# Kernel optimization log

Measured on AMD Instinct MI355X. Metric: run time of the kernel, lower is better.

Reference implementation:

```python
import jax, jax.numpy as jnp
import numpy as np

N, E = 16384, 524288
IN_C, H1, H2 = 128, 128, 64
EDGE_F = 16
NB = 10                      # binary outputs
MC_GROUPS = (4, 6)           # multi-class group sizes (proto, service)
NC = 10                      # continuous outputs
EPS = 1e-5


def setup_inputs() -> dict:
    key = jax.random.key(0)
    ks = jax.random.split(key, 16)
    def lin(k, fan_in, fan_out):
        s = 1.0 / np.sqrt(fan_in)
        kw, kb = jax.random.split(k)
        return (jax.random.uniform(kw, (fan_in, fan_out), jnp.float32, -s, s),
                jax.random.uniform(kb, (fan_out,), jnp.float32, -s, s))
    w1, b1 = lin(ks[0], IN_C, H1)
    w2, b2 = lin(ks[1], H1, H2)
    w_bin, b_bin = lin(ks[2], H2, NB)
    w_mc, b_mc = lin(ks[3], H2, sum(MC_GROUPS))
    w_cont, b_cont = lin(ks[4], H2, NC)
    w_edge, b_edge = lin(ks[5], 2 * H2, EDGE_F)
    return {
        "x": jax.random.normal(ks[6], (N, IN_C), jnp.float32),
        "edge_index": jax.random.randint(ks[7], (2, E), 0, N, jnp.int64),
        "edge_attr": jax.random.normal(ks[8], (E, EDGE_F), jnp.float32),
        "w1": w1, "b1": b1,
        "bn1_g": jnp.ones((H1,), jnp.float32), "bn1_b": jnp.zeros((H1,), jnp.float32),
        "w2": w2, "b2": b2,
        "bn2_g": jnp.ones((H2,), jnp.float32), "bn2_b": jnp.zeros((H2,), jnp.float32),
        "w_bin": w_bin, "b_bin": b_bin,
        "w_mc": w_mc, "b_mc": b_mc,
        "w_cont": w_cont, "b_cont": b_cont,
        "w_edge": w_edge, "b_edge": b_edge,
    }


def _gcn(x, w, b, src, dst, norm, n):
    # GCNConv: x' = D^-1/2 (A+I) D^-1/2 (x W) + b
    h = x @ w
    msg = h[src] * norm[:, None]
    agg = jax.ops.segment_sum(msg, dst, num_segments=n)
    return agg + b


def _bn(h, g, b):
    m = jnp.mean(h, axis=0)
    v = jnp.var(h, axis=0)
    return g * (h - m) * jax.lax.rsqrt(v + EPS) + b


def reference(x, edge_index, edge_attr, w1, b1, bn1_g, bn1_b, w2, b2, bn2_g, bn2_b,
              w_bin, b_bin, w_mc, b_mc, w_cont, b_cont, w_edge, b_edge):
    n = x.shape[0]
    loops = jnp.arange(n, dtype=edge_index.dtype)
    src = jnp.concatenate([edge_index[0], loops])
    dst = jnp.concatenate([edge_index[1], loops])
    deg = jax.ops.segment_sum(jnp.ones_like(src, dtype=x.dtype), dst, num_segments=n)
    dis = jax.lax.rsqrt(deg)  # deg >= 1 thanks to self-loops
    norm = dis[src] * dis[dst]

    h = jax.nn.relu(_bn(_gcn(x, w1, b1, src, dst, norm, n), bn1_g, bn1_b))
    z = jax.nn.relu(_bn(_gcn(h, w2, b2, src, dst, norm, n), bn2_g, bn2_b))

    # node feature reconstruction: [binary sigmoid | per-group softmax | continuous]
    binary = jax.nn.sigmoid(z @ w_bin + b_bin)
    mc_logits = z @ w_mc + b_mc
    mc_parts, s = [], 0
    for g in MC_GROUPS:
        mc_parts.append(jax.nn.softmax(mc_logits[:, s:s + g], axis=1))
        s += g
    cont = z @ w_cont + b_cont
    reconstructed_x = jnp.concatenate([binary] + mc_parts + [cont], axis=1)

    adj = z @ z.T  # [N, N]

    edge_emb = jnp.concatenate([z[edge_index[0]], z[edge_index[1]]], axis=1)
    edge_features = edge_emb @ w_edge + b_edge
    return (reconstructed_x, adj, edge_features)
```

## Files before the change

### kernel.cpp

```cpp
#include <hip/hip_runtime.h>
#include <hip/hip_bf16.h>
#include <math.h>


constexpr int kN = 16384;
constexpr int kE = 524288;
constexpr float kEps = 1e-5f;

typedef __attribute__((ext_vector_type(8))) short short8v;
typedef __attribute__((ext_vector_type(4))) float f32x4;

__device__ inline float bf2f(unsigned short u) {
  return __uint_as_float(((unsigned)u) << 16);
}
__device__ inline unsigned short f2bf(float f) {
  unsigned u = __float_as_uint(f);
  return (unsigned short)((u + 0x7fff + ((u >> 16) & 1)) >> 16);
}

__global__ void zero_kernel(int* counts, float* sums1, float* sums2,
                            const float* __restrict__ we, __hip_bfloat16* wfr) {
  int i = blockIdx.x * 256 + threadIdx.x;
  if (i < kN) counts[i] = 0;
  if (i < 256) sums1[i] = 0.f;
  if (i < 128) sums2[i] = 0.f;
  if (i < 2048) {
    int f = i >> 9, l = (i >> 3) & 63, j = i & 7;
    int lr = l & 15, lg = l >> 4;
    int krow = f * 32 + lg * 8 + j;
    wfr[i] = __float2bfloat16(we[krow * 16 + lr]);
  }
}

__global__ void hist_kernel(const int* __restrict__ dst, int* __restrict__ counts) {
  int e = blockIdx.x * 256 + threadIdx.x;
  if (e < kE) atomicAdd(&counts[dst[e]], 1);
}

__global__ __launch_bounds__(1024) void scan_kernel(const int* __restrict__ counts,
    int* __restrict__ offsets, int* __restrict__ pos, float* __restrict__ dis) {
  __shared__ int wave_tot[16];
  int tid = threadIdx.x;
  int base = tid * 16;
  int loc[16];
  int s = 0;
#pragma unroll
  for (int i = 0; i < 16; i++) { loc[i] = s; s += counts[base + i]; }
  int lane = tid & 63, wv = tid >> 6;
  int incl = s;
#pragma unroll
  for (int d = 1; d < 64; d <<= 1) {
    int v = __shfl_up(incl, d, 64);
    if (lane >= d) incl += v;
  }
  if (lane == 63) wave_tot[wv] = incl;
  __syncthreads();
  int woff = 0;
  for (int i = 0; i < wv; i++) woff += wave_tot[i];
  int excl = woff + incl - s;
#pragma unroll
  for (int i = 0; i < 16; i++) {
    int o = excl + loc[i];
    offsets[base + i] = o;
    pos[base + i] = o;
    dis[base + i] = rsqrtf((float)counts[base + i] + 1.0f);
  }
}

__global__ void fill_kernel(const int* __restrict__ src, const int* __restrict__ dst,
                            int* __restrict__ pos, int* __restrict__ csr_src) {
  int e = blockIdx.x * 256 + threadIdx.x;
  if (e < kE) {
    int d = dst[e];
    int p = atomicAdd(&pos[d], 1);
    csr_src[p] = src[e];
  }
}

__global__ __launch_bounds__(256) void gemm1_kernel(
    const float* __restrict__ A, const float* __restrict__ W,
    const float* __restrict__ dis, __hip_bfloat16* __restrict__ out) {
  constexpr int BC = 128, NJ = 8, WF4 = 4;
  __shared__ float xs[64 * 33];
  __shared__ float wsh[32 * BC];
  int tid = threadIdx.x;
  int tx = tid & 15, ty = tid >> 4;
  int r0 = blockIdx.x * 64;
  float acc[4][NJ];
#pragma unroll
  for (int r = 0; r < 4; r++)
#pragma unroll
    for (int j = 0; j < NJ; j++) acc[r][j] = 0.f;

  for (int kb = 0; kb < 128; kb += 32) {
    __syncthreads();
#pragma unroll
    for (int q = 0; q < 2; q++) {
      int f = tid + q * 256;
      int row = f >> 3, kq = f & 7;
      float4 v = *(const float4*)(A + (size_t)(r0 + row) * 128 + kb + kq * 4);
      int bb = row * 33 + kq * 4;
      xs[bb + 0] = v.x; xs[bb + 1] = v.y; xs[bb + 2] = v.z; xs[bb + 3] = v.w;
    }
#pragma unroll
    for (int q = 0; q < WF4; q++) {
      int f = tid + q * 256;
      int k = f / (BC / 4), cq = f % (BC / 4);
      *(float4*)&wsh[k * BC + cq * 4] =
          *(const float4*)(W + (size_t)(kb + k) * BC + cq * 4);
    }
    __syncthreads();
#pragma unroll
    for (int kk = 0; kk < 32; kk++) {
      float av[4];
#pragma unroll
      for (int r = 0; r < 4; r++) av[r] = xs[(ty * 4 + r) * 33 + kk];
#pragma unroll
      for (int j = 0; j < NJ; j++) {
        float bv = wsh[kk * BC + tx + j * 16];
#pragma unroll
        for (int r = 0; r < 4; r++) acc[r][j] = fmaf(av[r], bv, acc[r][j]);
      }
    }
  }
#pragma unroll
  for (int r = 0; r < 4; r++) {
    int row = r0 + ty * 4 + r;
    float dr = dis[row];
#pragma unroll
    for (int j = 0; j < NJ; j++)
      out[(size_t)row * BC + tx + j * 16] = __float2bfloat16(acc[r][j] * dr);
  }
}

__global__ __launch_bounds__(256) void gemm2_kernel(
    const unsigned short* __restrict__ A, const float* __restrict__ W,
    const float* __restrict__ sums, const float* __restrict__ g,
    const float* __restrict__ b, const float* __restrict__ dis,
    __hip_bfloat16* __restrict__ out) {
  constexpr int BC = 64, NJ = 4, WF4 = 2;
  __shared__ float xs[64 * 33];
  __shared__ float wsh[32 * BC];
  __shared__ float s_scl[128], s_shf[128];
  int tid = threadIdx.x;
  if (tid < 128) {
    float mean = sums[tid] / (float)kN;
    float var = sums[128 + tid] / (float)kN - mean * mean;
    float inv = rsqrtf(var + kEps);
    float sc = g[tid] * inv;
    s_scl[tid] = sc;
    s_shf[tid] = b[tid] - mean * sc;
  }
  int tx = tid & 15, ty = tid >> 4;
  int r0 = blockIdx.x * 64;
  float acc[4][NJ];
#pragma unroll
  for (int r = 0; r < 4; r++)
#pragma unroll
    for (int j = 0; j < NJ; j++) acc[r][j] = 0.f;

  for (int kb = 0; kb < 128; kb += 32) {
    __syncthreads();
    {
      int row = tid >> 2, kq = tid & 3;
      short8v v8 = *(const short8v*)(A + (size_t)(r0 + row) * 128 + kb + kq * 8);
      int bb = row * 33 + kq * 8;
#pragma unroll
      for (int j = 0; j < 8; j++) {
        int c = kb + kq * 8 + j;
        float v = bf2f((unsigned short)v8[j]);
        xs[bb + j] = fmaxf(0.f, fmaf(v, s_scl[c], s_shf[c]));
      }
    }
#pragma unroll
    for (int q = 0; q < WF4; q++) {
      int f = tid + q * 256;
      int k = f / (BC / 4), cq = f % (BC / 4);
      *(float4*)&wsh[k * BC + cq * 4] =
          *(const float4*)(W + (size_t)(kb + k) * BC + cq * 4);
    }
    __syncthreads();
#pragma unroll
    for (int kk = 0; kk < 32; kk++) {
      float av[4];
#pragma unroll
      for (int r = 0; r < 4; r++) av[r] = xs[(ty * 4 + r) * 33 + kk];
#pragma unroll
      for (int j = 0; j < NJ; j++) {
        float bv = wsh[kk * BC + tx + j * 16];
#pragma unroll
        for (int r = 0; r < 4; r++) acc[r][j] = fmaf(av[r], bv, acc[r][j]);
      }
    }
  }
#pragma unroll
  for (int r = 0; r < 4; r++) {
    int row = r0 + ty * 4 + r;
    float dr = dis[row];
#pragma unroll
    for (int j = 0; j < NJ; j++)
      out[(size_t)row * BC + tx + j * 16] = __float2bfloat16(acc[r][j] * dr);
  }
}

__global__ __launch_bounds__(256) void agg1_kernel(const unsigned short* __restrict__ hs,
    const int* __restrict__ csr_src, const int* __restrict__ offsets,
    const int* __restrict__ counts, const float* __restrict__ dis,
    unsigned short* __restrict__ t1) {
  int tid = threadIdx.x;
  int wv = tid >> 6, lane = tid & 63;
  int d = blockIdx.x * 4 + wv;
  int g = lane >> 4, l = lane & 15;
  float acc[8];
  if (g == 0) {
    short8v v = *(const short8v*)(hs + (size_t)d * 128 + l * 8);
#pragma unroll
    for (int j = 0; j < 8; j++) acc[j] = bf2f((unsigned short)v[j]);
  } else {
#pragma unroll
    for (int j = 0; j < 8; j++) acc[j] = 0.f;
  }
  int s0 = offsets[d], n = counts[d];
  int i = g;
  for (; i + 4 < n; i += 8) {
    int sa = csr_src[s0 + i];
    int sb = csr_src[s0 + i + 4];
    short8v va = *(const short8v*)(hs + (size_t)sa * 128 + l * 8);
    short8v vb = *(const short8v*)(hs + (size_t)sb * 128 + l * 8);
#pragma unroll
    for (int j = 0; j < 8; j++) acc[j] += bf2f((unsigned short)va[j]);
#pragma unroll
    for (int j = 0; j < 8; j++) acc[j] += bf2f((unsigned short)vb[j]);
  }
  if (i < n) {
    int sa = csr_src[s0 + i];
    short8v va = *(const short8v*)(hs + (size_t)sa * 128 + l * 8);
#pragma unroll
    for (int j = 0; j < 8; j++) acc[j] += bf2f((unsigned short)va[j]);
  }
#pragma unroll
  for (int j = 0; j < 8; j++) {
    acc[j] += __shfl_xor(acc[j], 16, 64);
    acc[j] += __shfl_xor(acc[j], 32, 64);
  }
  if (g == 0) {
    float dd = dis[d];
    short8v o;
#pragma unroll
    for (int j = 0; j < 8; j++) o[j] = (short)f2bf(acc[j] * dd);
    *(short8v*)(t1 + (size_t)d * 128 + l * 8) = o;
  }
}

__global__ __launch_bounds__(256) void agg2_kernel(const unsigned short* __restrict__ hs,
    const int* __restrict__ csr_src, const int* __restrict__ offsets,
    const int* __restrict__ counts, const float* __restrict__ dis,
    float* __restrict__ t2) {
  int tid = threadIdx.x;
  int wv = tid >> 6, lane = tid & 63;
  int d = blockIdx.x * 4 + wv;
  int g = lane >> 3, l = lane & 7;
  float acc[8];
  if (g == 0) {
    short8v v = *(const short8v*)(hs + (size_t)d * 64 + l * 8);
#pragma unroll
    for (int j = 0; j < 8; j++) acc[j] = bf2f((unsigned short)v[j]);
  } else {
#pragma unroll
    for (int j = 0; j < 8; j++) acc[j] = 0.f;
  }
  int s0 = offsets[d], n = counts[d];
  int i = g;
  for (; i + 8 < n; i += 16) {
    int sa = csr_src[s0 + i];
    int sb = csr_src[s0 + i + 8];
    short8v va = *(const short8v*)(hs + (size_t)sa * 64 + l * 8);
    short8v vb = *(const short8v*)(hs + (size_t)sb * 64 + l * 8);
#pragma unroll
    for (int j = 0; j < 8; j++) acc[j] += bf2f((unsigned short)va[j]);
#pragma unroll
    for (int j = 0; j < 8; j++) acc[j] += bf2f((unsigned short)vb[j]);
  }
  if (i < n) {
    int sa = csr_src[s0 + i];
    short8v va = *(const short8v*)(hs + (size_t)sa * 64 + l * 8);
#pragma unroll
    for (int j = 0; j < 8; j++) acc[j] += bf2f((unsigned short)va[j]);
  }
#pragma unroll
  for (int j = 0; j < 8; j++) {
    acc[j] += __shfl_xor(acc[j], 8, 64);
    acc[j] += __shfl_xor(acc[j], 16, 64);
    acc[j] += __shfl_xor(acc[j], 32, 64);
  }
  if (g == 0) {
    float dd = dis[d];
    float* o = t2 + (size_t)d * 64 + l * 8;
    f32x4 o0 = {acc[0] * dd, acc[1] * dd, acc[2] * dd, acc[3] * dd};
    f32x4 o1 = {acc[4] * dd, acc[5] * dd, acc[6] * dd, acc[7] * dd};
    *(f32x4*)o = o0;
    *(f32x4*)(o + 4) = o1;
  }
}

template <int C, bool BF16>
__global__ __launch_bounds__(256) void stats_kernel(const void* __restrict__ t,
                                                    float* __restrict__ sums) {
  constexpr int RP = 256 / C;
  int c = threadIdx.x % C;
  int rr = threadIdx.x / C;
  float s = 0.f, s2 = 0.f;
  for (int r = blockIdx.x * RP + rr; r < kN; r += gridDim.x * RP) {
    float v;
    if constexpr (BF16) v = bf2f(((const unsigned short*)t)[(size_t)r * C + c]);
    else v = ((const float*)t)[(size_t)r * C + c];
    s += v;
    s2 += v * v;
  }
  atomicAdd(&sums[c], s);
  atomicAdd(&sums[C + c], s2);
}

__global__ __launch_bounds__(256) void zheads_kernel(const float* __restrict__ t2,
    const float* __restrict__ sums, const float* __restrict__ gg,
    const float* __restrict__ bb2,
    const float* __restrict__ wbin, const float* __restrict__ bbin,
    const float* __restrict__ wmc, const float* __restrict__ bmc,
    const float* __restrict__ wcont, const float* __restrict__ bcont,
    float* __restrict__ out0, unsigned short* __restrict__ zb) {
  __shared__ float wT[30 * 64];
  __shared__ float bias[32];
  __shared__ float s_scl[64], s_shf[64];
  int tid = threadIdx.x;
  for (int idx = tid; idx < 1920; idx += 256) {
    int j = idx >> 6, k = idx & 63;
    const float* src = (j < 10) ? wbin : (j < 20) ? wmc : wcont;
    wT[idx] = src[k * 10 + (j % 10)];
  }
  if (tid < 30)
    bias[tid] = (tid < 10) ? bbin[tid] : (tid < 20) ? bmc[tid - 10] : bcont[tid - 20];
  if (tid < 64) {
    float mean = sums[tid] / (float)kN;
    float var = sums[64 + tid] / (float)kN - mean * mean;
    float inv = rsqrtf(var + kEps);
    float sc = gg[tid] * inv;
    s_scl[tid] = sc;
    s_shf[tid] = bb2[tid] - mean * sc;
  }
  __syncthreads();
  int n = blockIdx.x * 256 + tid;
  float zr[64];
  const float4* t4 = (const float4*)(t2 + (size_t)n * 64);
#pragma unroll
  for (int q = 0; q < 16; q++) {
    float4 v = t4[q];
    zr[4 * q + 0] = fmaxf(0.f, fmaf(v.x, s_scl[4 * q + 0], s_shf[4 * q + 0]));
    zr[4 * q + 1] = fmaxf(0.f, fmaf(v.y, s_scl[4 * q + 1], s_shf[4 * q + 1]));
    zr[4 * q + 2] = fmaxf(0.f, fmaf(v.z, s_scl[4 * q + 2], s_shf[4 * q + 2]));
    zr[4 * q + 3] = fmaxf(0.f, fmaf(v.w, s_scl[4 * q + 3], s_shf[4 * q + 3]));
  }
  unsigned short* zrow = zb + (size_t)n * 64;
#pragma unroll
  for (int q = 0; q < 8; q++) {
    short8v o;
#pragma unroll
    for (int j = 0; j < 8; j++) o[j] = (short)f2bf(zr[q * 8 + j]);
    *(short8v*)(zrow + q * 8) = o;
  }
  float acc[30];
#pragma unroll
  for (int j = 0; j < 30; j++) {
    float s = bias[j];
#pragma unroll
    for (int kc = 0; kc < 16; kc++) {
      f32x4 wv = *(const f32x4*)&wT[j * 64 + kc * 4];
      s = fmaf(zr[4 * kc + 0], wv.x, s);
      s = fmaf(zr[4 * kc + 1], wv.y, s);
      s = fmaf(zr[4 * kc + 2], wv.z, s);
      s = fmaf(zr[4 * kc + 3], wv.w, s);
    }
    acc[j] = s;
  }
  float* o = out0 + (size_t)n * 30;
#pragma unroll
  for (int j = 0; j < 10; j++) o[j] = 1.f / (1.f + expf(-acc[j]));
  float m1 = fmaxf(fmaxf(acc[10], acc[11]), fmaxf(acc[12], acc[13]));
  float e1[4], s1 = 0.f;
#pragma unroll
  for (int j = 0; j < 4; j++) { e1[j] = expf(acc[10 + j] - m1); s1 += e1[j]; }
#pragma unroll
  for (int j = 0; j < 4; j++) o[10 + j] = e1[j] / s1;
  float m2 = acc[14];
#pragma unroll
  for (int j = 15; j < 20; j++) m2 = fmaxf(m2, acc[j]);
  float e2[6], s2 = 0.f;
#pragma unroll
  for (int j = 0; j < 6; j++) { e2[j] = expf(acc[14 + j] - m2); s2 += e2[j]; }
#pragma unroll
  for (int j = 0; j < 6; j++) o[14 + j] = e2[j] / s2;
#pragma unroll
  for (int j = 0; j < 10; j++) o[20 + j] = acc[20 + j];
}

__global__ __launch_bounds__(256) void adjedge_kernel(const short* __restrict__ zb,
    const int* __restrict__ srcs, const int* __restrict__ dsts,
    const short* __restrict__ wfr, const float* __restrict__ be,
    float* __restrict__ adj, float* __restrict__ eout) {
  __shared__ float cs[128 * 132];
  int tid = threadIdx.x;
  int wid = tid >> 6, lane = tid & 63;
  int lr = lane & 15, lg = lane >> 4;

  if (blockIdx.x < 1024) {
    float* es = &cs[wid * 256];
    int gw = blockIdx.x * 4 + wid;
    short8v bfr[4];
#pragma unroll
    for (int f = 0; f < 4; f++)
      bfr[f] = *(const short8v*)(wfr + ((size_t)f * 64 + lane) * 8);
    float bias = be[lr];
    for (int t = 0; t < 8; t++) {
      int e0 = (gw * 8 + t) * 16;
      int se = srcs[e0 + lr], de = dsts[e0 + lr];
      short8v a0 = *(const short8v*)(zb + (size_t)se * 64 + lg * 8);
      short8v a1 = *(const short8v*)(zb + (size_t)se * 64 + 32 + lg * 8);
      short8v a2 = *(const short8v*)(zb + (size_t)de * 64 + lg * 8);
      short8v a3 = *(const short8v*)(zb + (size_t)de * 64 + 32 + lg * 8);
      f32x4 acc = {0.f, 0.f, 0.f, 0.f};
      acc = __builtin_amdgcn_mfma_f32_16x16x32_bf16(a0, bfr[0], acc, 0, 0, 0);
      acc = __builtin_amdgcn_mfma_f32_16x16x32_bf16(a1, bfr[1], acc, 0, 0, 0);
      acc = __builtin_amdgcn_mfma_f32_16x16x32_bf16(a2, bfr[2], acc, 0, 0, 0);
      acc = __builtin_amdgcn_mfma_f32_16x16x32_bf16(a3, bfr[3], acc, 0, 0, 0);
#pragma unroll
      for (int r = 0; r < 4; r++)
        es[(lg * 4 + r) * 16 + lr] = acc[r] + bias;
      f32x4 v = *(const f32x4*)&es[lane * 4];
      *(f32x4*)(eout + (size_t)e0 * 16 + lane * 4) = v;
    }
    return;
  }

  int bid = blockIdx.x - 1024;
  int li0 = (wid >> 1) * 64;
  int lj0 = (wid & 1) * 64;
  int i0 = (bid & 127) * 128 + li0;
  int j0 = (bid >> 7) * 128 + lj0;
  short8v a[4][2], b[4][2];
#pragma unroll
  for (int mt = 0; mt < 4; mt++)
#pragma unroll
    for (int ks = 0; ks < 2; ks++)
      a[mt][ks] = *(const short8v*)(zb + (size_t)(i0 + mt * 16 + lr) * 64 + ks * 32 + lg * 8);
#pragma unroll
  for (int nt = 0; nt < 4; nt++)
#pragma unroll
    for (int ks = 0; ks < 2; ks++)
      b[nt][ks] = *(const short8v*)(zb + (size_t)(j0 + nt * 16 + lr) * 64 + ks * 32 + lg * 8);
  f32x4 acc[4][4];
#pragma unroll
  for (int mt = 0; mt < 4; mt++)
#pragma unroll
    for (int nt = 0; nt < 4; nt++) {
      f32x4 zz = {0.f, 0.f, 0.f, 0.f};
      acc[mt][nt] = zz;
    }
#pragma unroll
  for (int ks = 0; ks < 2; ks++)
#pragma unroll
    for (int mt = 0; mt < 4; mt++)
#pragma unroll
      for (int nt = 0; nt < 4; nt++)
        acc[mt][nt] = __builtin_amdgcn_mfma_f32_16x16x32_bf16(a[mt][ks], b[nt][ks],
                                                              acc[mt][nt], 0, 0, 0);
#pragma unroll
  for (int mt = 0; mt < 4; mt++)
#pragma unroll
    for (int nt = 0; nt < 4; nt++)
#pragma unroll
      for (int r = 0; r < 4; r++)
        cs[(li0 + mt * 16 + lg * 4 + r) * 132 + lj0 + nt * 16 + lr] = acc[mt][nt][r];
  __syncthreads();
  int row = tid >> 5;
  int c4 = tid & 31;
  size_t gbase = (size_t)((bid & 127) * 128 + row) * kN + (bid >> 7) * 128 + c4 * 4;
  const float* lbase = &cs[row * 132 + c4 * 4];
#pragma unroll
  for (int it = 0; it < 16; it++) {
    f32x4 v = *(const f32x4*)(lbase + it * 8 * 132);
    *(f32x4*)(adj + gbase + (size_t)it * 8 * kN) = v;
  }
}

extern "C" void kernel_launch(void* const* d_in, const int* in_sizes, int n_in,
                              void* d_out, int out_size, void* d_ws, size_t ws_size,
                              hipStream_t stream) {
  const float* x      = (const float*)d_in[0];
  const int*   ei     = (const int*)d_in[1];
  const float* w1     = (const float*)d_in[3];
  const float* bn1_g  = (const float*)d_in[5];
  const float* bn1_b  = (const float*)d_in[6];
  const float* w2     = (const float*)d_in[7];
  const float* bn2_g  = (const float*)d_in[9];
  const float* bn2_b  = (const float*)d_in[10];
  const float* w_bin  = (const float*)d_in[11];
  const float* b_bin  = (const float*)d_in[12];
  const float* w_mc   = (const float*)d_in[13];
  const float* b_mc   = (const float*)d_in[14];
  const float* w_cont = (const float*)d_in[15];
  const float* b_cont = (const float*)d_in[16];
  const float* w_edge = (const float*)d_in[17];
  const float* b_edge = (const float*)d_in[18];

  float* out0 = (float*)d_out;
  float* adj  = out0 + (size_t)kN * 30;
  float* eout = adj + (size_t)kN * kN;

  char* wp = (char*)d_ws;
  auto alloc = [&](size_t bytes) {
    char* p = wp;
    wp += (bytes + 255) & ~(size_t)255;
    return p;
  };
  int*   counts  = (int*)alloc((size_t)kN * 4);
  int*   offsets = (int*)alloc((size_t)kN * 4);
  int*   pos     = (int*)alloc((size_t)kN * 4);
  int*   csr_src = (int*)alloc((size_t)kE * 4);
  float* dis     = (float*)alloc((size_t)kN * 4);
  float* sums1   = (float*)alloc(256 * 4);
  float* sums2   = (float*)alloc(128 * 4);
  unsigned short* hs1 = (unsigned short*)alloc((size_t)kN * 128 * 2);
  unsigned short* t1  = (unsigned short*)alloc((size_t)kN * 128 * 2);
  unsigned short* hs2 = (unsigned short*)alloc((size_t)kN * 64 * 2);
  float* t2      = (float*)alloc((size_t)kN * 64 * 4);
  unsigned short* zb  = (unsigned short*)alloc((size_t)kN * 64 * 2);
  __hip_bfloat16* wfr = (__hip_bfloat16*)alloc(2048 * 2);

  const int* esrc = ei;
  const int* edst = ei + kE;

  zero_kernel<<<dim3(64), dim3(256), 0, stream>>>(counts, sums1, sums2, w_edge, wfr);
  hist_kernel<<<dim3(2048), dim3(256), 0, stream>>>(edst, counts);
  scan_kernel<<<dim3(1), dim3(1024), 0, stream>>>(counts, offsets, pos, dis);
  fill_kernel<<<dim3(2048), dim3(256), 0, stream>>>(esrc, edst, pos, csr_src);

  gemm1_kernel<<<dim3(kN / 64), dim3(256), 0, stream>>>(
      x, w1, dis, (__hip_bfloat16*)hs1);
  agg1_kernel<<<dim3(kN / 4), dim3(256), 0, stream>>>(
      hs1, csr_src, offsets, counts, dis, t1);
  stats_kernel<128, true><<<dim3(256), dim3(256), 0, stream>>>(t1, sums1);

  gemm2_kernel<<<dim3(kN / 64), dim3(256), 0, stream>>>(
      t1, w2, sums1, bn1_g, bn1_b, dis, (__hip_bfloat16*)hs2);
  agg2_kernel<<<dim3(kN / 4), dim3(256), 0, stream>>>(
      hs2, csr_src, offsets, counts, dis, t2);
  stats_kernel<64, false><<<dim3(256), dim3(256), 0, stream>>>(t2, sums2);

  zheads_kernel<<<dim3(kN / 256), dim3(256), 0, stream>>>(
      t2, sums2, bn2_g, bn2_b, w_bin, b_bin, w_mc, b_mc, w_cont, b_cont, out0, zb);

  adjedge_kernel<<<dim3(1024 + 16384), dim3(256), 0, stream>>>(
      (const short*)zb, esrc, edst, (const short*)wfr, b_edge, adj, eout);
}
```

Before: 421.5 us.

## Shrink adj tile LDS staging to 32-row chunks to raise occupancy

The adj/edge kernel now stages the 128x128 output tile through LDS in four 32-row chunks instead of one full 128-row buffer. This cuts shared memory per block by about four times, and the kernel adds launch_bounds(256,4) so more blocks can stay resident per CU. The bf16 operand loads also move inside the k-loop to shorten register lifetimes. The trade-off is extra __syncthreads barriers per tile and serialised chunk writes, and the occupancy hint may squeeze registers.

Measured after the change: 544.9 us. +29.3%, slower.

```diff
diff --git a/kernel.cpp b/kernel.cpp
--- a/kernel.cpp
+++ b/kernel.cpp
@@ -402,11 +402,11 @@
   for (int j = 0; j < 10; j++) o[20 + j] = acc[20 + j];
 }
 
-__global__ __launch_bounds__(256) void adjedge_kernel(const short* __restrict__ zb,
+__global__ __launch_bounds__(256, 4) void adjedge_kernel(const short* __restrict__ zb,
     const int* __restrict__ srcs, const int* __restrict__ dsts,
     const short* __restrict__ wfr, const float* __restrict__ be,
     float* __restrict__ adj, float* __restrict__ eout) {
-  __shared__ float cs[128 * 132];
+  __shared__ float cs[32 * 132];
   int tid = threadIdx.x;
   int wid = tid >> 6, lane = tid & 63;
   int lr = lane & 15, lg = lane >> 4;
@@ -441,21 +441,11 @@
   }
 
   int bid = blockIdx.x - 1024;
+  int brow = bid & 127, bcol = bid >> 7;
   int li0 = (wid >> 1) * 64;
   int lj0 = (wid & 1) * 64;
-  int i0 = (bid & 127) * 128 + li0;
-  int j0 = (bid >> 7) * 128 + lj0;
-  short8v a[4][2], b[4][2];
-#pragma unroll
-  for (int mt = 0; mt < 4; mt++)
-#pragma unroll
-    for (int ks = 0; ks < 2; ks++)
-      a[mt][ks] = *(const short8v*)(zb + (size_t)(i0 + mt * 16 + lr) * 64 + ks * 32 + lg * 8);
-#pragma unroll
-  for (int nt = 0; nt < 4; nt++)
-#pragma unroll
-    for (int ks = 0; ks < 2; ks++)
-      b[nt][ks] = *(const short8v*)(zb + (size_t)(j0 + nt * 16 + lr) * 64 + ks * 32 + lg * 8);
+  int i0 = brow * 128 + li0;
+  int j0 = bcol * 128 + lj0;
   f32x4 acc[4][4];
 #pragma unroll
   for (int mt = 0; mt < 4; mt++)
@@ -465,29 +455,45 @@
       acc[mt][nt] = zz;
     }
 #pragma unroll
-  for (int ks = 0; ks < 2; ks++)
+  for (int ks = 0; ks < 2; ks++) {
+    short8v a[4], b[4];
 #pragma unroll
     for (int mt = 0; mt < 4; mt++)
+      a[mt] = *(const short8v*)(zb + (size_t)(i0 + mt * 16 + lr) * 64 + ks * 32 + lg * 8);
+#pragma unroll
+    for (int nt = 0; nt < 4; nt++)
+      b[nt] = *(const short8v*)(zb + (size_t)(j0 + nt * 16 + lr) * 64 + ks * 32 + lg * 8);
+#pragma unroll
+    for (int mt = 0; mt < 4; mt++)
 #pragma unroll
       for (int nt = 0; nt < 4; nt++)
-        acc[mt][nt] = __builtin_amdgcn_mfma_f32_16x16x32_bf16(a[mt][ks], b[nt][ks],
+        acc[mt][nt] = __builtin_amdgcn_mfma_f32_16x16x32_bf16(a[mt], b[nt],
                                                               acc[mt][nt], 0, 0, 0);
-#pragma unroll
-  for (int mt = 0; mt < 4; mt++)
-#pragma unroll
-    for (int nt = 0; nt < 4; nt++)
-#pragma unroll
-      for (int r = 0; r < 4; r++)
-        cs[(li0 + mt * 16 + lg * 4 + r) * 132 + lj0 + nt * 16 + lr] = acc[mt][nt][r];
-  __syncthreads();
-  int row = tid >> 5;
-  int c4 = tid & 31;
-  size_t gbase = (size_t)((bid & 127) * 128 + row) * kN + (bid >> 7) * 128 + c4 * 4;
-  const float* lbase = &cs[row * 132 + c4 * 4];
-#pragma unroll
-  for (int it = 0; it < 16; it++) {
-    f32x4 v = *(const f32x4*)(lbase + it * 8 * 132);
-    *(f32x4*)(adj + gbase + (size_t)it * 8 * kN) = v;
+  }
+#pragma unroll
+  for (int c = 0; c < 4; c++) {
+    int mtbase = 2 * c - (wid >> 1) * 4;
+    if (mtbase >= 0 && mtbase < 4) {
+#pragma unroll
+      for (int mm = 0; mm < 2; mm++) {
+        int mt = mtbase + mm;
+#pragma unroll
+        for (int nt = 0; nt < 4; nt++)
+#pragma unroll
+          for (int r = 0; r < 4; r++)
+            cs[(li0 + mt * 16 + lg * 4 + r - 32 * c) * 132 + lj0 + nt * 16 + lr] =
+                acc[mt][nt][r];
+      }
+    }
+    __syncthreads();
+#pragma unroll
+    for (int q = 0; q < 4; q++) {
+      int idx = q * 256 + tid;
+      int row = idx >> 5, c4 = idx & 31;
+      f32x4 v = *(const f32x4*)&cs[row * 132 + c4 * 4];
+      *(f32x4*)(adj + (size_t)(brow * 128 + c * 32 + row) * kN + bcol * 128 + c4 * 4) = v;
+    }
+    __syncthreads();
   }
 }
 
```
